# Optimization experiments

Hardware: AMD Instinct MI355X
Metric: run time of the kernel (lower is better)

## Reference

```python
import jax, jax.numpy as jnp
import numpy as np

NUM_HEADS = 8
D_HEAD = 64
LN_EPS = 1e-6


def _pad_idx(lengths, max_len):
    # flat indices into a [B*max_len, ...] dense buffer for each packed token
    return np.concatenate([b * max_len + np.arange(int(l)) for b, l in enumerate(lengths)])


def _layer_norm(x, scale, bias):
    mu = jnp.mean(x, axis=-1, keepdims=True)
    var = jnp.mean(jnp.square(x - mu), axis=-1, keepdims=True)
    return (x - mu) * jax.lax.rsqrt(var + LN_EPS) * scale + bias


def setup_inputs() -> dict:
    key = jax.random.key(0)
    ks = jax.random.split(key, 12)
    d_model, d_ff, H, dh = 512, 2048, NUM_HEADS, D_HEAD
    lengths = np.array([128 * (i + 1) for i in range(8)], dtype=np.int64)  # sum = 4608
    total = int(lengths.sum())
    s = 0.02
    return {
        "x": jax.random.normal(ks[0], (total, d_model), jnp.float32),
        "mem": jax.random.normal(ks[1], (total, d_model), jnp.float32),
        "lengths_x": lengths,
        "lengths_mem": lengths.copy(),
        "Wq": jax.random.normal(ks[2], (d_model, H * dh), jnp.float32) * s,
        "Wk": jax.random.normal(ks[3], (d_model, H * dh), jnp.float32) * s,
        "Wv": jax.random.normal(ks[4], (d_model, H * dh), jnp.float32) * s,
        "Wo": jax.random.normal(ks[5], (H * dh, d_model), jnp.float32) * s,
        "ln1_scale": jnp.ones((d_model,), jnp.float32),
        "ln1_bias": jnp.zeros((d_model,), jnp.float32),
        "W1": jax.random.normal(ks[6], (d_model, d_ff), jnp.float32) * s,
        "b1": jnp.zeros((d_ff,), jnp.float32),
        "W2": jax.random.normal(ks[7], (d_ff, d_model), jnp.float32) * s,
        "b2": jnp.zeros((d_model,), jnp.float32),
        "ln2_scale": jnp.ones((d_model,), jnp.float32),
        "ln2_bias": jnp.zeros((d_model,), jnp.float32),
    }


def reference(x, mem, lengths_x, lengths_mem, Wq, Wk, Wv, Wo,
              ln1_scale, ln1_bias, W1, b1, W2, b2, ln2_scale, ln2_bias):
    lx = np.asarray(lengths_x)
    lm = np.asarray(lengths_mem)
    B = lx.shape[0]
    Lx = int(lx.max())
    Lm = int(lm.max())
    H, dh = NUM_HEADS, D_HEAD

    idx_x = _pad_idx(lx, Lx)
    idx_m = _pad_idx(lm, Lm)

    def pad(packed, idx, B, L):
        dense = jnp.zeros((B * L,) + packed.shape[1:], packed.dtype).at[idx].set(packed)
        return dense.reshape((B, L) + packed.shape[1:])

    q = pad((x @ Wq).reshape(-1, H, dh), idx_x, B, Lx)   # [B, Lx, H, dh]
    k = pad((mem @ Wk).reshape(-1, H, dh), idx_m, B, Lm)  # [B, Lm, H, dh]
    v = pad((mem @ Wv).reshape(-1, H, dh), idx_m, B, Lm)

    e = jnp.einsum('bxhd,byhd->bhxy', q, k) / np.sqrt(dh)  # [B, H, Lx, Lm]
    # validity mask: (query pos < len_x) & (key pos < len_mem)
    mask = (np.arange(Lx)[None, :, None] < lx[:, None, None]) & \
           (np.arange(Lm)[None, None, :] < lm[:, None, None])
    mask = jnp.asarray(mask)[:, None, :, :]  # [B, 1, Lx, Lm]
    e = jnp.where(mask, e, jnp.float32(-1e30))  # finite -inf surrogate; identical softmax on valid rows
    alpha = jax.nn.softmax(e, axis=-1)
    out = jnp.einsum('bhxy,byhd->bxhd', alpha, v).reshape(B, Lx, H * dh)
    out = out @ Wo                                  # [B, Lx, d_model]
    out = out.reshape(B * Lx, -1)[idx_x]            # pack back to [total_x, d_model]

    h = _layer_norm(x + out, ln1_scale, ln1_bias)
    ffn = jax.nn.relu(h @ W1 + b1) @ W2 + b2
    return _layer_norm(h + ffn, ln2_scale, ln2_bias)
```

## Files before the change

kernel.cpp:

```cpp
#include <hip/hip_runtime.h>
#include <stdint.h>

typedef short bf8v __attribute__((ext_vector_type(8)));
typedef float f4v  __attribute__((ext_vector_type(4)));
typedef short s8v  __attribute__((ext_vector_type(8)));
typedef short s4v  __attribute__((ext_vector_type(4)));
typedef int   i2v  __attribute__((ext_vector_type(2)));

__device__ __forceinline__ float bf2f(short b){
  unsigned u = ((unsigned)(unsigned short)b) << 16;
  union { unsigned u; float f; } c; c.u = u; return c.f;
}
__device__ __forceinline__ short f2bf(float f){
  union { float f; unsigned u; } c; c.f = f;
  unsigned r = (c.u + 0x7FFFu + ((c.u >> 16) & 1u)) >> 16;
  return (short)r;
}
__device__ __forceinline__ void gload16(const short* g, short* l){
  __builtin_amdgcn_global_load_lds(
      (const __attribute__((address_space(1))) void*)g,
      (__attribute__((address_space(3))) void*)l, 16, 0, 0);
}

__global__ void prep_kernel(const int* lx, const int* lm, int* meta){
  __shared__ int sjp[9], skvc[8];
  int tid = threadIdx.x;
  if (tid == 0){
    int is64 = ((lx[1] | lx[3] | lx[5] | lx[7]) == 0) ? 1 : 0;
    int ox = 0, om = 0;
    for (int b = 0; b < 8; ++b){
      int a = is64 ? lx[2*b] : lx[b];
      int c = is64 ? lm[2*b] : lm[b];
      meta[b] = a; meta[8+b] = c;
      meta[16+b] = ox; meta[25+b] = om;
      ox += a; om += c;
    }
    meta[24] = ox; meta[33] = om;
    int jp = 0;
    for (int b = 0; b < 8; ++b){
      int Lm_ = meta[8+b];
      int kvc = (Lm_ + 255) / 256; if (kvc > 4) kvc = 4; if (kvc < 1) kvc = 1;
      int clen = (((Lm_ + kvc - 1) / kvc) + 31) & ~31;
      meta[34+b] = kvc; meta[42+b] = clen;
      meta[50+b] = jp;
      sjp[b] = jp; skvc[b] = kvc;
      int qt = (meta[b] + 63) / 64;
      jp += qt * kvc * 8;
    }
    meta[58] = jp;
    sjp[8] = jp;
  }
  __syncthreads();
  int njobs = sjp[8];
  for (int j = tid; j < njobs; j += blockDim.x){
    int b = 0;
    #pragma unroll
    for (int i = 1; i < 8; ++i) if (j >= sjp[i]) b = i;
    int local = j - sjp[b];
    int kvc = skvc[b];
    int h = local & 7;
    int r = local >> 3;
    int c = r % kvc;
    int qt = r / kvc;
    meta[64+j] = b | (h << 4) | (c << 7) | (qt << 11);
  }
}

__global__ __launch_bounds__(256) void cvt2bf(const float* __restrict__ x,
                                              const float* __restrict__ mem,
                                              short* __restrict__ xb,
                                              short* __restrict__ mb,
                                              long long n){
  long long t = (long long)blockIdx.x * 256 + threadIdx.x;
  long long i = t * 8;
  const float* s; short* d;
  if (i < n){ s = x + i; d = xb + i; }
  else {
    i -= n; if (i >= n) return;
    s = mem + i; d = mb + i;
  }
  float4 f0 = *(const float4*)s;
  float4 f1 = *(const float4*)(s + 4);
  s8v o;
  o[0]=f2bf(f0.x); o[1]=f2bf(f0.y); o[2]=f2bf(f0.z); o[3]=f2bf(f0.w);
  o[4]=f2bf(f1.x); o[5]=f2bf(f1.y); o[6]=f2bf(f1.z); o[7]=f2bf(f1.w);
  *(s8v*)d = o;
}

__global__ __launch_bounds__(256) void cvt_w_t(
    const float* __restrict__ Wq, const float* __restrict__ Wk,
    const float* __restrict__ Wv, const float* __restrict__ Wo,
    const float* __restrict__ W1, const float* __restrict__ W2,
    short* __restrict__ WqT, short* __restrict__ WkT,
    short* __restrict__ WvT, short* __restrict__ WoT,
    short* __restrict__ W1T, short* __restrict__ W2T){
  __shared__ float tile[32][33];
  int bid = blockIdx.x;
  const float* W; short* WT; int K, N, t0;
  if      (bid <  256){ W=Wq; WT=WqT; K=512;  N=512;  t0=0;    }
  else if (bid <  512){ W=Wk; WT=WkT; K=512;  N=512;  t0=256;  }
  else if (bid <  768){ W=Wv; WT=WvT; K=512;  N=512;  t0=512;  }
  else if (bid < 1024){ W=Wo; WT=WoT; K=512;  N=512;  t0=768;  }
  else if (bid < 2048){ W=W1; WT=W1T; K=512;  N=2048; t0=1024; }
  else                { W=W2; WT=W2T; K=2048; N=512;  t0=2048; }
  int lt = bid - t0;
  int ntn = N / 32;
  int tk = lt / ntn, tn = lt % ntn;
  int r0 = threadIdx.x >> 5, c = threadIdx.x & 31;
  #pragma unroll
  for (int i = 0; i < 4; ++i){
    int r = r0 + i*8;
    tile[r][c] = W[(long)(tk*32 + r)*N + tn*32 + c];
  }
  __syncthreads();
  #pragma unroll
  for (int i = 0; i < 4; ++i){
    int r = r0 + i*8;
    WT[(long)(tn*32 + r)*K + tk*32 + c] = f2bf(tile[c][r]);
  }
}

template<int BM>
__device__ __forceinline__ void stage_gemm(const short* A, const short* Bt,
    long brow, long bcol, int M, int N, int K, int t,
    short* Als, short* Bls){
  int tid = threadIdx.x;
  #pragma unroll
  for (int i = 0; i < BM/64; ++i){
    int cc = i*256 + tid;
    int row = cc >> 2, slot = cc & 3;
    int cg = slot ^ ((row >> 1) & 3);
    long ar = brow + row; if (ar >= M) ar = M - 1;
    gload16(A + ar*(long)K + t + cg*8, &Als[cc*8]);
  }
  #pragma unroll
  for (int i = 0; i < 2; ++i){
    int cc = i*256 + tid;
    int row = cc >> 2, slot = cc & 3;
    int cg = slot ^ ((row >> 1) & 3);
    long br = bcol + row; if (br >= N) br = N - 1;
    gload16(Bt + br*(long)K + t + cg*8, &Bls[cc*8]);
  }
}

template<int BM>
__device__ __forceinline__ void gemm_core(const short* A, const short* Bt,
    short* __restrict__ C, const float* __restrict__ bias,
    int M, int N, int K, float scale, int relu, int colmajor,
    long brow, long bcol, short* Als, short* Bls){
  constexpr int NREP = (BM == 128) ? 4 : 2;
  int tid = threadIdx.x;
  int lane = tid & 63, w = tid >> 6;
  int wrow = (BM == 128) ? (w >> 1) * 64 : 0;
  int wcol = (BM == 128) ? (w & 1) * 64 : w * 32;
  int l15 = lane & 15, l4 = lane >> 4;

  f4v acc[4][NREP];
  #pragma unroll
  for (int m = 0; m < 4; ++m)
    #pragma unroll
    for (int n = 0; n < NREP; ++n) acc[m][n] = (f4v){0.f,0.f,0.f,0.f};

  int nt = K / 32;
  stage_gemm<BM>(A, Bt, brow, bcol, M, N, K, 0, Als, Bls);
  for (int t = 0; t < nt; ++t){
    __syncthreads();
    if (t + 1 < nt)
      stage_gemm<BM>(A, Bt, brow, bcol, M, N, K, (t+1)*32,
                     Als + ((t+1)&1)*(BM*32), Bls + ((t+1)&1)*4096);
    const short* Ab = Als + (t&1)*(BM*32);
    const short* Bb = Bls + (t&1)*4096;
    bf8v a[4], b[NREP];
    #pragma unroll
    for (int m = 0; m < 4; ++m){
      int row = wrow + m*16 + l15;
      int slot = l4 ^ ((row >> 1) & 3);
      a[m] = *(const bf8v*)&Ab[row*32 + slot*8];
    }
    #pragma unroll
    for (int n = 0; n < NREP; ++n){
      int row = wcol + n*16 + l15;
      int slot = l4 ^ ((row >> 1) & 3);
      b[n] = *(const bf8v*)&Bb[row*32 + slot*8];
    }
    #pragma unroll
    for (int m = 0; m < 4; ++m)
      #pragma unroll
      for (int n = 0; n < NREP; ++n)
        acc[m][n] = __builtin_amdgcn_mfma_f32_16x16x32_bf16(a[m], b[n], acc[m][n], 0, 0, 0);
  }

  #pragma unroll
  for (int m = 0; m < 4; ++m){
    #pragma unroll
    for (int n = 0; n < NREP; ++n){
      long col = bcol + wcol + n*16 + l15;
      float bi = (bias != nullptr && col < N) ? bias[col] : 0.f;
      #pragma unroll
      for (int j = 0; j < 4; ++j){
        long row = brow + wrow + m*16 + 4*l4 + j;
        if (row < M && col < N){
          float v = acc[m][n][j] * scale + bi;
          if (relu) v = fmaxf(v, 0.f);
          C[colmajor ? (col*(long)M + row) : (row*(long)N + col)] = f2bf(v);
        }
      }
    }
  }
}

__global__ __launch_bounds__(256) void gemm_bt(
    const short* __restrict__ A, const short* __restrict__ Bt,
    short* __restrict__ C, const float* __restrict__ bias,
    int M, int N, int K, float scale, int relu, int colmajor){
  __shared__ __align__(16) short Als[2*128*32];
  __shared__ __align__(16) short Bls[2*128*32];
  gemm_core<128>(A, Bt, C, bias, M, N, K, scale, relu, colmajor,
                 (long)blockIdx.y * 128, (long)blockIdx.x * 128, Als, Bls);
}

__global__ __launch_bounds__(256) void gemm_bt64(
    const short* __restrict__ A, const short* __restrict__ Bt,
    short* __restrict__ C, const float* __restrict__ bias,
    int M, int N, int K, float scale, int relu, int colmajor){
  __shared__ __align__(16) short Als[2*64*32];
  __shared__ __align__(16) short Bls[2*128*32];
  gemm_core<64>(A, Bt, C, bias, M, N, K, scale, relu, colmajor,
                (long)blockIdx.y * 64, (long)blockIdx.x * 128, Als, Bls);
}

__global__ __launch_bounds__(256) void gemm_qkv(
    const short* __restrict__ xb, const short* __restrict__ mb,
    const short* __restrict__ WqT, const short* __restrict__ WkT,
    const short* __restrict__ WvT,
    short* __restrict__ Qb, short* __restrict__ Kbf, short* __restrict__ Vtb,
    int total){
  __shared__ __align__(16) short Als[2*64*32];
  __shared__ __align__(16) short Bls[2*128*32];
  int seg = blockIdx.x >> 2;
  const short* A  = (seg == 0) ? xb : mb;
  const short* Bt = (seg == 0) ? WqT : ((seg == 1) ? WkT : WvT);
  short* C        = (seg == 0) ? Qb  : ((seg == 1) ? Kbf : Vtb);
  float scale     = (seg == 0) ? 0.125f : 1.f;
  int colmajor    = (seg == 2);
  gemm_core<64>(A, Bt, C, nullptr, total, 512, 512, scale, 0, colmajor,
                (long)blockIdx.y * 64, (long)(blockIdx.x & 3) * 128, Als, Bls);
}

__global__ __launch_bounds__(256) void attn_kernel(
    const short* __restrict__ Q, const short* __restrict__ Kb,
    const short* __restrict__ Vt, short* __restrict__ Ob,
    short* __restrict__ Opart, float* __restrict__ mlpart,
    const int* __restrict__ meta, int total){
  __shared__ __align__(16) short Kls[2][32*64];
  __shared__ __align__(16) short Vls[2][64*32];
  __shared__ __align__(16) short Pls[4][16*32];
  int tid = threadIdx.x;
  int lane = tid & 63, w = tid >> 6;
  int l15 = lane & 15, l4 = lane >> 4;
  int njobs = meta[58];

  for (int j = blockIdx.x; j < njobs; j += gridDim.x){
    int word = meta[64+j];
    int b = word & 15, h = (word >> 4) & 7, c = (word >> 7) & 15, qt = word >> 11;
    int Lx = meta[b], Lm = meta[8+b];
    int ox = meta[16+b], om = meta[25+b];
    int kvc = meta[34+b], clen = meta[42+b];
    int c0 = c * clen;
    int cend = c0 + clen; if (cend > Lm) cend = Lm;
    int nt = (cend - c0 + 31) / 32;
    int qbase = qt*64 + w*16;

    __syncthreads();

    #define ATTN_STAGE(T, BUF)                                                  \
      {                                                                         \
        int kv0_ = c0 + (T)*32;                                                 \
        int kr = tid >> 3, ks_ = tid & 7;                                       \
        int cgk = ks_ ^ (kr & 7);                                               \
        int ktok = kv0_ + kr; if (ktok >= Lm) ktok = Lm - 1;                    \
        gload16(Kb + (long)(om + ktok)*512 + h*64 + cgk*8, &Kls[BUF][tid*8]);   \
        int vr = tid >> 2, vs = tid & 3;                                        \
        int cgv = vs ^ (vr & 3);                                                \
        int vkv = kv0_ + cgv*8; if (vkv + 8 > Lm) vkv = Lm - 8;                 \
        gload16(Vt + (long)(h*64 + vr)*total + om + vkv, &Vls[BUF][tid*8]);     \
      }

    ATTN_STAGE(0, 0)

    int qr = qbase + l15;
    const short* qp = Q + (long)(ox + (qr < Lx ? qr : Lx - 1))*512 + h*64 + l4*8;
    bf8v aq0 = *(const bf8v*)qp;
    bf8v aq1 = *(const bf8v*)(qp + 32);

    float mrun = -1e30f, lrun = 0.f;
    f4v o[4];
    #pragma unroll
    for (int n = 0; n < 4; ++n) o[n] = (f4v){0.f,0.f,0.f,0.f};

    for (int t = 0; t < nt; ++t){
      __syncthreads();
      if (t + 1 < nt) ATTN_STAGE(t+1, (t+1)&1)
      int buf = t & 1;
      int kv0 = c0 + t*32;

      f4v s[2];
      #pragma unroll
      for (int n = 0; n < 2; ++n){
        int krow = n*16 + l15;
        bf8v k0 = *(const bf8v*)&Kls[buf][krow*64 + ((l4    ) ^ (krow & 7))*8];
        bf8v k1 = *(const bf8v*)&Kls[buf][krow*64 + ((4 + l4) ^ (krow & 7))*8];
        f4v z = (f4v){0.f,0.f,0.f,0.f};
        z = __builtin_amdgcn_mfma_f32_16x16x32_bf16(k0, aq0, z, 0, 0, 0);
        z = __builtin_amdgcn_mfma_f32_16x16x32_bf16(k1, aq1, z, 0, 0, 0);
        s[n] = z;
      }
      if (kv0 + 32 > cend){
        #pragma unroll
        for (int n = 0; n < 2; ++n){
          int kvb = kv0 + n*16 + 4*l4;
          #pragma unroll
          for (int jj = 0; jj < 4; ++jj)
            if (kvb + jj >= cend) s[n][jj] = -1e30f;
        }
      }
      float m1 = fmaxf(fmaxf(fmaxf(s[0][0], s[0][1]), fmaxf(s[0][2], s[0][3])),
                       fmaxf(fmaxf(s[1][0], s[1][1]), fmaxf(s[1][2], s[1][3])));
      m1 = fmaxf(m1, __shfl_xor(m1, 16, 64));
      m1 = fmaxf(m1, __shfl_xor(m1, 32, 64));
      float mnew = fmaxf(mrun, m1);
      float sc = __expf(mrun - mnew);
      mrun = mnew;
      float rs = 0.f;
      #pragma unroll
      for (int n = 0; n < 2; ++n)
        #pragma unroll
        for (int jj = 0; jj < 4; ++jj){
          float p = __expf(s[n][jj] - mnew);
          s[n][jj] = p; rs += p;
        }
      rs += __shfl_xor(rs, 16, 64);
      rs += __shfl_xor(rs, 32, 64);
      lrun = lrun * sc + rs;
      #pragma unroll
      for (int n = 0; n < 4; ++n) o[n] *= sc;

      #pragma unroll
      for (int n = 0; n < 2; ++n){
        unsigned r0, r1;
        asm("v_cvt_pk_bf16_f32 %0, %1, %2" : "=v"(r0) : "v"(s[n][0]), "v"(s[n][1]));
        asm("v_cvt_pk_bf16_f32 %0, %1, %2" : "=v"(r1) : "v"(s[n][2]), "v"(s[n][3]));
        i2v pr; pr[0] = (int)r0; pr[1] = (int)r1;
        int cs = (n*4 + l4) ^ ((l15 & 3) << 1);
        *(i2v*)&Pls[w][l15*32 + cs*4] = pr;
      }
      bf8v pb = *(const bf8v*)&Pls[w][l15*32 + (((2*l4) ^ ((l15 & 3) << 1))*4)];

      #pragma unroll
      for (int n2 = 0; n2 < 4; ++n2){
        int vrow = n2*16 + l15;
        bf8v vv = *(const bf8v*)&Vls[buf][vrow*32 + ((l4 ^ (vrow & 3))*8)];
        o[n2] = __builtin_amdgcn_mfma_f32_16x16x32_bf16(vv, pb, o[n2], 0, 0, 0);
      }
    }
    #undef ATTN_STAGE

    if (qr < Lx){
      if (kvc == 1){
        float inv = 1.f / lrun;
        long obase = (long)(ox + qr)*512 + h*64;
        #pragma unroll
        for (int n2 = 0; n2 < 4; ++n2){
          s4v ov;
          #pragma unroll
          for (int jj = 0; jj < 4; ++jj) ov[jj] = f2bf(o[n2][jj] * inv);
          *(s4v*)&Ob[obase + n2*16 + l4*4] = ov;
        }
      } else {
        long slot = ((long)(ox + qr)*8 + h)*4 + c;
        #pragma unroll
        for (int n2 = 0; n2 < 4; ++n2){
          s4v ov;
          #pragma unroll
          for (int jj = 0; jj < 4; ++jj) ov[jj] = f2bf(o[n2][jj]);
          *(s4v*)&Opart[slot*64 + n2*16 + l4*4] = ov;
        }
        if (l4 == 0){
          float2 ml; ml.x = mrun; ml.y = lrun;
          *(float2*)&mlpart[slot*2] = ml;
        }
      }
    }
  }
}

__global__ __launch_bounds__(256) void attn_combine(
    const short* __restrict__ Opart, const float* __restrict__ mlpart,
    short* __restrict__ Ob, const int* __restrict__ meta, int total){
  int w = threadIdx.x >> 6, lane = threadIdx.x & 63;
  int row = blockIdx.x*4 + w;
  if (row >= total) return;
  int b = 0;
  #pragma unroll
  for (int i = 1; i < 8; ++i) if (row >= meta[16+i]) b = i;
  int kvc = meta[34+b];
  if (kvc <= 1) return;
  for (int h = 0; h < 8; ++h){
    long sbase = ((long)row*8 + h)*4;
    float m_ = -1e30f;
    for (int c = 0; c < kvc; ++c) m_ = fmaxf(m_, mlpart[(sbase+c)*2]);
    float num = 0.f, den = 0.f;
    for (int c = 0; c < kvc; ++c){
      float mc = mlpart[(sbase+c)*2];
      float lc = mlpart[(sbase+c)*2 + 1];
      float wgt = __expf(mc - m_);
      num += wgt * bf2f(Opart[(sbase+c)*64 + lane]);
      den += wgt * lc;
    }
    Ob[(long)row*512 + h*64 + lane] = f2bf(num / den);
  }
}

__global__ __launch_bounds__(256) void ln_fuse(
    const float* __restrict__ Af, const short* __restrict__ Ab,
    const short* __restrict__ Bb,
    const float* __restrict__ gamma, const float* __restrict__ beta,
    short* __restrict__ outb, float* __restrict__ outf, int rows){
  int w = threadIdx.x >> 6, lane = threadIdx.x & 63;
  long row = (long)blockIdx.x * 4 + w;
  if (row >= rows) return;
  int c0 = lane * 8;
  long base = row * 512 + c0;
  float v[8];
  if (Af){
    float4 f0 = *(const float4*)(Af + base);
    float4 f1 = *(const float4*)(Af + base + 4);
    v[0]=f0.x; v[1]=f0.y; v[2]=f0.z; v[3]=f0.w;
    v[4]=f1.x; v[5]=f1.y; v[6]=f1.z; v[7]=f1.w;
  } else {
    s8v a = *(const s8v*)(Ab + base);
    #pragma unroll
    for (int j = 0; j < 8; ++j) v[j] = bf2f(a[j]);
  }
  s8v bb = *(const s8v*)(Bb + base);
  #pragma unroll
  for (int j = 0; j < 8; ++j) v[j] += bf2f(bb[j]);
  float sum = 0.f;
  #pragma unroll
  for (int j = 0; j < 8; ++j) sum += v[j];
  #pragma unroll
  for (int m = 1; m < 64; m <<= 1) sum += __shfl_xor(sum, m, 64);
  float mu = sum * (1.f/512.f);
  float q = 0.f;
  #pragma unroll
  for (int j = 0; j < 8; ++j){ float d = v[j] - mu; q += d*d; }
  #pragma unroll
  for (int m = 1; m < 64; m <<= 1) q += __shfl_xor(q, m, 64);
  float rs = rsqrtf(q * (1.f/512.f) + 1e-6f);
  float ov[8];
  #pragma unroll
  for (int j = 0; j < 8; ++j)
    ov[j] = (v[j] - mu) * rs * gamma[c0 + j] + beta[c0 + j];
  if (outb){
    s8v os;
    #pragma unroll
    for (int j = 0; j < 8; ++j) os[j] = f2bf(ov[j]);
    *(s8v*)(outb + base) = os;
  } else {
    float4 f0 = {ov[0], ov[1], ov[2], ov[3]};
    float4 f1 = {ov[4], ov[5], ov[6], ov[7]};
    *(float4*)(outf + base) = f0;
    *(float4*)(outf + base + 4) = f1;
  }
}

extern "C" void kernel_launch(void* const* d_in, const int* in_sizes, int n_in,
                              void* d_out, int out_size, void* d_ws, size_t ws_size,
                              hipStream_t stream){
  (void)n_in; (void)out_size; (void)ws_size;
  const float* x   = (const float*)d_in[0];
  const float* mem = (const float*)d_in[1];
  const int*   lxr = (const int*)d_in[2];
  const int*   lmr = (const int*)d_in[3];
  const float* Wq  = (const float*)d_in[4];
  const float* Wk  = (const float*)d_in[5];
  const float* Wv  = (const float*)d_in[6];
  const float* Wo  = (const float*)d_in[7];
  const float* g1  = (const float*)d_in[8];
  const float* be1 = (const float*)d_in[9];
  const float* W1  = (const float*)d_in[10];
  const float* b1  = (const float*)d_in[11];
  const float* W2  = (const float*)d_in[12];
  const float* b2  = (const float*)d_in[13];
  const float* g2  = (const float*)d_in[14];
  const float* be2 = (const float*)d_in[15];
  float* out = (float*)d_out;

  int total = in_sizes[0] / 512;
  if (total <= 0) return;
  long long n = (long long)total * 512;

  char* p = (char*)d_ws;
  int*   meta = (int*)p;    p += 16384;
  short* xb   = (short*)p;  p += n*2;
  short* mb   = (short*)p;  p += n*2;
  short* Qb   = (short*)p;  p += n*2;
  short* Kbf  = (short*)p;  p += n*2;
  short* Vtb  = (short*)p;  p += n*2;
  short* attnb= (short*)p;  p += n*2;
  short* woout= (short*)p;  p += n*2;
  short* hb   = (short*)p;  p += n*2;
  short* ffn1 = (short*)p;  p += (long long)total*2048*2;
  short* ffn2 = (short*)p;  p += n*2;
  short* WqT  = (short*)p;  p += 512*512*2;
  short* WkT  = (short*)p;  p += 512*512*2;
  short* WvT  = (short*)p;  p += 512*512*2;
  short* WoT  = (short*)p;  p += 512*512*2;
  short* W1T  = (short*)p;  p += 2048*512*2;
  short* W2T  = (short*)p;  p += 512*2048*2;

  prep_kernel<<<1, 256, 0, stream>>>(lxr, lmr, meta);

  long long th = (2*n)/8;
  cvt2bf<<<dim3((unsigned)((th + 255)/256)), dim3(256), 0, stream>>>(x, mem, xb, mb, n);
  cvt_w_t<<<dim3(3072), dim3(256), 0, stream>>>(Wq,Wk,Wv,Wo,W1,W2, WqT,WkT,WvT,WoT,W1T,W2T);

  int mt128 = (total + 127)/128;
  int mt64  = (total + 63)/64;
  gemm_qkv<<<dim3(12, mt64), 256, 0, stream>>>(xb, mb, WqT, WkT, WvT, Qb, Kbf, Vtb, total);

  attn_kernel<<<dim3(2048), 256, 0, stream>>>(Qb, Kbf, Vtb, attnb,
                                              ffn1, (float*)woout, meta, total);
  attn_combine<<<dim3((unsigned)((total + 3)/4)), 256, 0, stream>>>(
      ffn1, (const float*)woout, attnb, meta, total);

  gemm_bt64<<<dim3(4, mt64), 256, 0, stream>>>(attnb, WoT, woout, nullptr, total, 512, 512, 1.f, 0, 0);
  ln_fuse<<<dim3((unsigned)((total + 3)/4)), 256, 0, stream>>>(x, nullptr, woout, g1, be1, hb, nullptr, total);

  gemm_bt<<<dim3(16, mt128), 256, 0, stream>>>(hb,   W1T, ffn1, b1, total, 2048, 512,  1.f, 1, 0);
  gemm_bt64<<<dim3(4, mt64), 256, 0, stream>>>(ffn1, W2T, ffn2, b2, total, 512,  2048, 1.f, 0, 0);
  ln_fuse<<<dim3((unsigned)((total + 3)/4)), 256, 0, stream>>>(nullptr, hb, ffn2, g2, be2, nullptr, out, total);
}
```

Before: 179.4 us.

## Split-K the Wo and W2 GEMMs with fp32 partials reduced in LayerNorm

```diff
diff --git a/kernel.cpp b/kernel.cpp
--- a/kernel.cpp
+++ b/kernel.cpp
@@ -120,14 +120,12 @@
   }
 }
 
-template<int BM>
-__device__ __forceinline__ void stage_gemm(const short* A, const short* Bt,
+__device__ __forceinline__ void stage_g64(const short* A, const short* Bt,
     long brow, long bcol, int M, int N, int K, int t,
     short* Als, short* Bls){
   int tid = threadIdx.x;
-  #pragma unroll
-  for (int i = 0; i < BM/64; ++i){
-    int cc = i*256 + tid;
+  {
+    int cc = tid;
     int row = cc >> 2, slot = cc & 3;
     int cg = slot ^ ((row >> 1) & 3);
     long ar = brow + row; if (ar >= M) ar = M - 1;
@@ -143,42 +141,41 @@
   }
 }
 
-template<int BM>
-__device__ __forceinline__ void gemm_core(const short* A, const short* Bt,
-    short* __restrict__ C, const float* __restrict__ bias,
-    int M, int N, int K, float scale, int relu, int colmajor,
+__device__ __forceinline__ void gemm_core64(const short* A, const short* Bt,
+    short* __restrict__ Cb, float* __restrict__ Cf,
+    const float* __restrict__ bias,
+    int M, int N, int K, int k0, int klen,
+    float scale, int relu, int colmajor,
     long brow, long bcol, short* Als, short* Bls){
-  constexpr int NREP = (BM == 128) ? 4 : 2;
   int tid = threadIdx.x;
   int lane = tid & 63, w = tid >> 6;
-  int wrow = (BM == 128) ? (w >> 1) * 64 : 0;
-  int wcol = (BM == 128) ? (w & 1) * 64 : w * 32;
+  int wcol = w * 32;
   int l15 = lane & 15, l4 = lane >> 4;
 
-  f4v acc[4][NREP];
+  f4v acc[4][2];
   #pragma unroll
   for (int m = 0; m < 4; ++m)
     #pragma unroll
-    for (int n = 0; n < NREP; ++n) acc[m][n] = (f4v){0.f,0.f,0.f,0.f};
-
-  int nt = K / 32;
-  stage_gemm<BM>(A, Bt, brow, bcol, M, N, K, 0, Als, Bls);
+    for (int n = 0; n < 2; ++n) acc[m][n] = (f4v){0.f,0.f,0.f,0.f};
+
+  int nt = klen / 32;
+  stage_g64(A, Bt, brow, bcol, M, N, K, k0, Als, Bls);
   for (int t = 0; t < nt; ++t){
     __syncthreads();
     if (t + 1 < nt)
-      stage_gemm<BM>(A, Bt, brow, bcol, M, N, K, (t+1)*32,
-                     Als + ((t+1)&1)*(BM*32), Bls + ((t+1)&1)*4096);
-    const short* Ab = Als + (t&1)*(BM*32);
+      stage_g64(A, Bt, brow, bcol, M, N, K, k0 + (t+1)*32,
+                Als + ((t+1)&1)*2048, Bls + ((t+1)&1)*4096);
+    const short* Ab = Als + (t&1)*2048;
     const short* Bb = Bls + (t&1)*4096;
-    bf8v a[4], b[NREP];
+    bf8v a[4], b[2];
     #pragma unroll
     for (int m = 0; m < 4; ++m){
-      int row = wrow + m*16 + l15;
+      int row = m*16 + l15;
       int slot = l4 ^ ((row >> 1) & 3);
       a[m] = *(const bf8v*)&Ab[row*32 + slot*8];
     }
     #pragma unroll
-    for (int n = 0; n < NREP; ++n){
+    for (int n = 0; n < 2; ++n){
       int row = wcol + n*16 + l15;
       int slot = l4 ^ ((row >> 1) & 3);
       b[n] = *(const bf8v*)&Bb[row*32 + slot*8];
@@ -186,47 +183,54 @@
     #pragma unroll
     for (int m = 0; m < 4; ++m)
       #pragma unroll
-      for (int n = 0; n < NREP; ++n)
+      for (int n = 0; n < 2; ++n)
         acc[m][n] = __builtin_amdgcn_mfma_f32_16x16x32_bf16(a[m], b[n], acc[m][n], 0, 0, 0);
   }
 
+  if (Cf){
+    #pragma unroll
+    for (int m = 0; m < 4; ++m)
+      #pragma unroll
+      for (int n = 0; n < 2; ++n){
+        long col = bcol + wcol + n*16 + l15;
+        #pragma unroll
+        for (int j = 0; j < 4; ++j){
+          long row = brow + m*16 + 4*l4 + j;
+          if (row < M && col < N) Cf[row*(long)N + col] = acc[m][n][j];
+        }
+      }
+    return;
+  }
   #pragma unroll
   for (int m = 0; m < 4; ++m){
     #pragma unroll
-    for (int n = 0; n < NREP; ++n){
+    for (int n = 0; n < 2; ++n){
       long col = bcol + wcol + n*16 + l15;
       float bi = (bias != nullptr && col < N) ? bias[col] : 0.f;
       #pragma unroll
       for (int j = 0; j < 4; ++j){
-        long row = brow + wrow + m*16 + 4*l4 + j;
+        long row = brow + m*16 + 4*l4 + j;
         if (row < M && col < N){
           float v = acc[m][n][j] * scale + bi;
           if (relu) v = fmaxf(v, 0.f);
-          C[colmajor ? (col*(long)M + row) : (row*(long)N + col)] = f2bf(v);
-        }
-      }
-    }
-  }
-}
-
-__global__ __launch_bounds__(256) void gemm_bt(
+          Cb[colmajor ? (col*(long)M + row) : (row*(long)N + col)] = f2bf(v);
+        }
+      }
+    }
+  }
+}
+
+__global__ __launch_bounds__(256) void gemm64(
     const short* __restrict__ A, const short* __restrict__ Bt,
-    short* __restrict__ C, const float* __restrict__ bias,
-    int M, int N, int K, float scale, int relu, int colmajor){
-  __shared__ __align__(16) short Als[2*128*32];
-  __shared__ __align__(16) short Bls[2*128*32];
-  gemm_core<128>(A, Bt, C, bias, M, N, K, scale, relu, colmajor,
-                 (long)blockIdx.y * 128, (long)blockIdx.x * 128, Als, Bls);
-}
-
-__global__ __launch_bounds__(256) void gemm_bt64(
-    const short* __restrict__ A, const short* __restrict__ Bt,
-    short* __restrict__ C, const float* __restrict__ bias,
-    int M, int N, int K, float scale, int relu, int colmajor){
+    short* __restrict__ Cb, float* __restrict__ Cf,
+    const float* __restrict__ bias,
+    int M, int N, int K, int klen, float scale, int relu, int colmajor){
   __shared__ __align__(16) short Als[2*64*32];
   __shared__ __align__(16) short Bls[2*128*32];
-  gemm_core<64>(A, Bt, C, bias, M, N, K, scale, relu, colmajor,
-                (long)blockIdx.y * 64, (long)blockIdx.x * 128, Als, Bls);
+  int chunk = blockIdx.z;
+  float* cf = Cf ? Cf + (long)chunk * M * N : nullptr;
+  gemm_core64(A, Bt, Cb, cf, bias, M, N, K, chunk*klen, klen, scale, relu, colmajor,
+              (long)blockIdx.y * 64, (long)blockIdx.x * 128, Als, Bls);
 }
 
 __global__ __launch_bounds__(256) void gemm_qkv(
@@ -243,8 +247,8 @@
   short* C        = (seg == 0) ? Qb  : ((seg == 1) ? Kbf : Vtb);
   float scale     = (seg == 0) ? 0.125f : 1.f;
   int colmajor    = (seg == 2);
-  gemm_core<64>(A, Bt, C, nullptr, total, 512, 512, scale, 0, colmajor,
-                (long)blockIdx.y * 64, (long)(blockIdx.x & 3) * 128, Als, Bls);
+  gemm_core64(A, Bt, C, nullptr, nullptr, total, 512, 512, 0, 512, scale, 0, colmajor,
+              (long)blockIdx.y * 64, (long)(blockIdx.x & 3) * 128, Als, Bls);
 }
 
 __global__ __launch_bounds__(256) void attn_kernel(
@@ -423,7 +427,8 @@
 
 __global__ __launch_bounds__(256) void ln_fuse(
     const float* __restrict__ Af, const short* __restrict__ Ab,
-    const short* __restrict__ Bb,
+    const float* __restrict__ Part, int nparts, long pstride,
+    const float* __restrict__ bias,
     const float* __restrict__ gamma, const float* __restrict__ beta,
     short* __restrict__ outb, float* __restrict__ outf, int rows){
   int w = threadIdx.x >> 6, lane = threadIdx.x & 63;
@@ -442,9 +447,17 @@
     #pragma unroll
     for (int j = 0; j < 8; ++j) v[j] = bf2f(a[j]);
   }
-  s8v bb = *(const s8v*)(Bb + base);
-  #pragma unroll
-  for (int j = 0; j < 8; ++j) v[j] += bf2f(bb[j]);
+  for (int c = 0; c < nparts; ++c){
+    const float* pp = Part + c*pstride + base;
+    float4 a0 = *(const float4*)pp;
+    float4 a1 = *(const float4*)(pp + 4);
+    v[0]+=a0.x; v[1]+=a0.y; v[2]+=a0.z; v[3]+=a0.w;
+    v[4]+=a1.x; v[5]+=a1.y; v[6]+=a1.z; v[7]+=a1.w;
+  }
+  if (bias){
+    #pragma unroll
+    for (int j = 0; j < 8; ++j) v[j] += bias[c0 + j];
+  }
   float sum = 0.f;
   #pragma unroll
   for (int j = 0; j < 8; ++j) sum += v[j];
@@ -466,7 +479,8 @@
     #pragma unroll
     for (int j = 0; j < 8; ++j) os[j] = f2bf(ov[j]);
     *(s8v*)(outb + base) = os;
-  } else {
+  }
+  if (outf){
     float4 f0 = {ov[0], ov[1], ov[2], ov[3]};
     float4 f1 = {ov[4], ov[5], ov[6], ov[7]};
     *(float4*)(outf + base) = f0;
@@ -511,7 +525,9 @@
   short* woout= (short*)p;  p += n*2;
   short* hb   = (short*)p;  p += n*2;
   short* ffn1 = (short*)p;  p += (long long)total*2048*2;
-  short* ffn2 = (short*)p;  p += n*2;
+  float* hf   = (float*)p;  p += n*4;
+  float* p_wo = (float*)p;  p += n*4*2;
+  float* p_ff = (float*)p;  p += n*4*4;
   short* WqT  = (short*)p;  p += 512*512*2;
   short* WkT  = (short*)p;  p += 512*512*2;
   short* WvT  = (short*)p;  p += 512*512*2;
@@ -525,8 +541,7 @@
   cvt2bf<<<dim3((unsigned)((th + 255)/256)), dim3(256), 0, stream>>>(x, mem, xb, mb, n);
   cvt_w_t<<<dim3(3072), dim3(256), 0, stream>>>(Wq,Wk,Wv,Wo,W1,W2, WqT,WkT,WvT,WoT,W1T,W2T);
 
-  int mt128 = (total + 127)/128;
-  int mt64  = (total + 63)/64;
+  int mt64 = (total + 63)/64;
   gemm_qkv<<<dim3(12, mt64), 256, 0, stream>>>(xb, mb, WqT, WkT, WvT, Qb, Kbf, Vtb, total);
 
   attn_kernel<<<dim3(2048), 256, 0, stream>>>(Qb, Kbf, Vtb, attnb,
@@ -534,10 +549,15 @@
   attn_combine<<<dim3((unsigned)((total + 3)/4)), 256, 0, stream>>>(
       ffn1, (const float*)woout, attnb, meta, total);
 
-  gemm_bt64<<<dim3(4, mt64), 256, 0, stream>>>(attnb, WoT, woout, nullptr, total, 512, 512, 1.f, 0, 0);
-  ln_fuse<<<dim3((unsigned)((total + 3)/4)), 256, 0, stream>>>(x, nullptr, woout, g1, be1, hb, nullptr, total);
-
-  gemm_bt<<<dim3(16, mt128), 256, 0, stream>>>(hb,   W1T, ffn1, b1, total, 2048, 512,  1.f, 1, 0);
-  gemm_bt64<<<dim3(4, mt64), 256, 0, stream>>>(ffn1, W2T, ffn2, b2, total, 512,  2048, 1.f, 0, 0);
-  ln_fuse<<<dim3((unsigned)((total + 3)/4)), 256, 0, stream>>>(nullptr, hb, ffn2, g2, be2, nullptr, out, total);
-}
+  gemm64<<<dim3(4, mt64, 2), 256, 0, stream>>>(attnb, WoT, nullptr, p_wo, nullptr,
+                                               total, 512, 512, 256, 1.f, 0, 0);
+  ln_fuse<<<dim3((unsigned)((total + 3)/4)), 256, 0, stream>>>(
+      x, nullptr, p_wo, 2, n, nullptr, g1, be1, hb, hf, total);
+
+  gemm64<<<dim3(16, mt64, 1), 256, 0, stream>>>(hb, W1T, ffn1, nullptr, b1,
+                                                total, 2048, 512, 512, 1.f, 1, 0);
+  gemm64<<<dim3(4, mt64, 4), 256, 0, stream>>>(ffn1, W2T, nullptr, p_ff, nullptr,
+                                               total, 512, 2048, 512, 1.f, 0, 0);
+  ln_fuse<<<dim3((unsigned)((total + 3)/4)), 256, 0, stream>>>(
+      hf, nullptr, p_ff, 4, n, b2, g2, be2, nullptr, out, total);
+}
```

Measured after the change: 180.5 us. Within noise of the previous version (+0.6%).
